# Performance work log

Measured on AMD Instinct MI355X. Metric: run time of the kernel, lower is better.

## Reference

```python
import jax, jax.numpy as jnp
import numpy as np

B, S, D, K, DF, H, DFF = 2, 512, 512, 8, 64, 8, 2048
DH = D // H  # d_head = 64
CS = D // K  # chunk_size = 64


def layer_norm(x, g, b, eps=1e-5):
    m = x.mean(-1, keepdims=True)
    v = ((x - m) ** 2).mean(-1, keepdims=True)
    return (x - m) / jnp.sqrt(v + eps) * g + b


def matexp_taylor(M, terms=6):
    # exp(M) ~= I + M + M^2/2! + ... (6 terms), batched over leading dims
    I = jnp.broadcast_to(jnp.eye(M.shape[-1], dtype=M.dtype), M.shape)
    res, P = I, I
    for n in range(1, terms + 1):
        P = jnp.matmul(P, M) / n
        res = res + P
    return res


def setup_inputs() -> dict:
    key = jax.random.key(0)
    ks = jax.random.split(key, 24)
    w = lambda k, shape, s=0.02: (jax.random.normal(k, shape, jnp.float32) * s)
    return {
        'x': jax.random.normal(ks[0], (B, S, D), jnp.float32),
        'u': jax.random.normal(ks[1], (B, S, DF), jnp.float32),
        'Wq': w(ks[2], (D, D)), 'bq': jnp.zeros((D,), jnp.float32),
        'Wk': w(ks[3], (D, D)), 'bk': jnp.zeros((D,), jnp.float32),
        'Wv': w(ks[4], (D, D)), 'bv': jnp.zeros((D,), jnp.float32),
        'Wo': w(ks[5], (D, D)), 'bo': jnp.zeros((D,), jnp.float32),
        'Wfp': w(ks[6], (DF, D)), 'bfp': jnp.zeros((D,), jnp.float32),
        'Wfo': w(ks[7], (D, DF)), 'bfo': jnp.zeros((DF,), jnp.float32),
        'Wc1': w(ks[8], (D, DFF)), 'bc1': jnp.zeros((DFF,), jnp.float32),
        'g_ln': jnp.ones((DFF,), jnp.float32), 'b_ln': jnp.zeros((DFF,), jnp.float32),
        # small scale keeps the Lie elements O(1) so the Taylor matexp is well-behaved
        'Wc2': w(ks[9], (DFF, D * K * K), 0.001), 'bc2': jnp.zeros((D * K * K,), jnp.float32),
    }


def reference(x, u, Wq, bq, Wk, bk, Wv, bv, Wo, bo, Wfp, bfp, Wfo, bfo,
              Wc1, bc1, g_ln, b_ln, Wc2, bc2):
    b, s, d = x.shape
    # --- ConnectionNetwork: A[b,s,d,k,k] ---
    h = jax.nn.gelu(x @ Wc1 + bc1, approximate=False)
    h = layer_norm(h, g_ln, b_ln)
    A = (h @ Wc2 + bc2).reshape(b, s, d, K, K)
    # --- ParallelTransport: lie[b,i,j] = sum_d (x_i - x_j)_d * A[j,d]  ---
    # (split into x_i.A_j and x_j.A_j terms to avoid [b,s,s,d,k,k] intermediate)
    lie = jnp.einsum('bid,bjdkl->bijkl', x, A) - jnp.einsum('bjd,bjdkl->bjkl', x, A)[:, None]
    Gamma = matexp_taylor(-lie)  # [b,s,s,k,k], Gamma[b,i,j] transports j->i
    # --- standard multi-head attention on x (eval mode, no dropout, no mask) ---
    q = (x @ Wq + bq).reshape(b, s, H, DH).transpose(0, 2, 1, 3)
    k_ = (x @ Wk + bk).reshape(b, s, H, DH).transpose(0, 2, 1, 3)
    v = (x @ Wv + bv).reshape(b, s, H, DH).transpose(0, 2, 1, 3)
    scores = jnp.einsum('bhid,bhjd->bhij', q, k_) / jnp.sqrt(jnp.float32(DH))
    attn = jax.nn.softmax(scores, axis=-1)
    ctx = jnp.einsum('bhij,bhjd->bhid', attn, v).transpose(0, 2, 1, 3).reshape(b, s, d)
    x_out = x + ctx @ Wo + bo
    # --- fiber transport: u_i += sum_j attn_avg[i,j] * Gamma[i,j] @ u_chunks[j] ---
    u_proj = u @ Wfp + bfp                      # [b,s,D]
    u_chunks = u_proj.reshape(b, s, K, CS)      # [b,s,k,cs]
    attn_avg = attn.mean(axis=1)                # [b,s,s]
    weighted = Gamma * attn_avg[..., None, None]
    u_t = jnp.einsum('bijkl,bjlc->bikc', weighted, u_chunks).reshape(b, s, d)
    u_out = u + u_t @ Wfo + bfo
    return (x_out, u_out)
```

## Files before the change

kernel.cpp:

```cpp
#include <hip/hip_runtime.h>
#include <math.h>

#define BB 2
#define SS 512
#define DD 512
#define HH 8
#define DFF 2048

typedef __attribute__((ext_vector_type(8))) short bf16x8;
typedef __attribute__((ext_vector_type(4))) float f32x4;

__device__ __forceinline__ float gelu_exact(float v) {
    return 0.5f * v * (1.0f + erff(v * 0.70710678118654752f));
}
__device__ __forceinline__ unsigned short f2bf(float f) {
    unsigned u = __float_as_uint(f);
    u += 0x7FFF + ((u >> 16) & 1);
    return (unsigned short)(u >> 16);
}
__device__ __forceinline__ float bf2f(unsigned short s) {
    return __uint_as_float(((unsigned)s) << 16);
}
__device__ __forceinline__ void gload16(const void* g, void* l) {
    __builtin_amdgcn_global_load_lds((const __attribute__((address_space(1))) void*)g,
                                     (__attribute__((address_space(3))) void*)l, 16, 0, 0);
}

template<int NT, int EPI>
__global__ __launch_bounds__(256)
void mgemm_k(const unsigned short* __restrict__ A, const unsigned short* __restrict__ B,
             const float* __restrict__ bias, const float* __restrict__ resid,
             float* __restrict__ Cf, unsigned short* __restrict__ Cb,
             int K, int lda, int ldb, int ldc, int batchH,
             long aSB, long aSH, long bSB, long bSH, long cSB, long cSH,
             float scale)
{
    __shared__ unsigned short As[128][32];
    __shared__ unsigned short Bs[NT][32];
    const int tid = threadIdx.x;
    const int wave = tid >> 6, lane = tid & 63;
    const int z = blockIdx.z;
    const int zb = z / batchH, zh = z % batchH;
    const unsigned short* Ab = A + (long)zb * aSB + (long)zh * aSH;
    const unsigned short* Bb = B + (long)zb * bSB + (long)zh * bSH;
    const int row0 = blockIdx.y * 128, col0 = blockIdx.x * NT;
    const int wm = wave >> 1, wn = wave & 1;
    const int lm = lane & 15, quad = lane >> 4;
    const int lrow = lane >> 2, lk = (lane & 3) * 8;
    constexpr int NTW = NT / 32;
    f32x4 acc[4][NTW];
    #pragma unroll
    for (int i = 0; i < 4; ++i)
        #pragma unroll
        for (int j = 0; j < NTW; ++j) acc[i][j] = (f32x4)0.f;

    for (int k0 = 0; k0 < K; k0 += 32) {
        #pragma unroll
        for (int t = 0; t < 2; ++t) {
            const int r = wave * 32 + t * 16;
            gload16(Ab + (long)(row0 + r + lrow) * lda + k0 + lk, &As[r][0]);
        }
        if (NT == 128) {
            #pragma unroll
            for (int t = 0; t < 2; ++t) {
                const int r = wave * 32 + t * 16;
                gload16(Bb + (long)(col0 + r + lrow) * ldb + k0 + lk, &Bs[r][0]);
            }
        } else {
            const int r = wave * 16;
            gload16(Bb + (long)(col0 + r + lrow) * ldb + k0 + lk, &Bs[r][0]);
        }
        __syncthreads();
        bf16x8 af[4], bfr[NTW];
        #pragma unroll
        for (int mt = 0; mt < 4; ++mt)
            af[mt] = *(const bf16x8*)&As[wm * 64 + mt * 16 + lm][quad * 8];
        #pragma unroll
        for (int nt = 0; nt < NTW; ++nt)
            bfr[nt] = *(const bf16x8*)&Bs[wn * (NT / 2) + nt * 16 + lm][quad * 8];
        #pragma unroll
        for (int mt = 0; mt < 4; ++mt)
            #pragma unroll
            for (int nt = 0; nt < NTW; ++nt)
                acc[mt][nt] = __builtin_amdgcn_mfma_f32_16x16x32_bf16(
                    af[mt], bfr[nt], acc[mt][nt], 0, 0, 0);
        __syncthreads();
    }
    float* Cfz = Cf ? Cf + (long)zb * cSB + (long)zh * cSH : nullptr;
    unsigned short* Cbz = Cb ? Cb + (long)zb * cSB + (long)zh * cSH : nullptr;
    #pragma unroll
    for (int mt = 0; mt < 4; ++mt) {
        #pragma unroll
        for (int nt = 0; nt < NTW; ++nt) {
            #pragma unroll
            for (int r = 0; r < 4; ++r) {
                const int row = row0 + wm * 64 + mt * 16 + quad * 4 + r;
                const int col = col0 + wn * (NT / 2) + nt * 16 + lm;
                float v = acc[mt][nt][r] * scale;
                if (EPI == 2)      v += bias[(col & 511) * 64 + (col >> 9)];
                else if (EPI == 1 || EPI == 4) v += bias[col];
                else if ((EPI == 3 || EPI == 5 || EPI == 6) && bias) v += bias[col];
                if (EPI == 1) v = gelu_exact(v);
                if (EPI == 4) v += resid[(long)row * ldc + col];
                if (EPI == 0 || EPI == 1 || EPI == 4)
                    Cfz[(long)row * ldc + col] = v;
                else if (EPI == 2 || EPI == 3)
                    Cbz[(long)row * ldc + col] = f2bf(v);
                else if (EPI == 5)
                    Cb[(long)(row >> 9) * 262144 + (col >> 6) * 32768 +
                       (col & 63) * 512 + (row & 511)] = f2bf(v);
                else if (EPI == 6)
                    Cb[(long)(row >> 9) * 262144 + (col & 63) * 4096 +
                       (row & 511) * 8 + (col >> 6)] = f2bf(v);
            }
        }
    }
}

__global__ __launch_bounds__(512, 2)
void fc2_k(const unsigned short* __restrict__ A, const unsigned short* __restrict__ Bm,
           const float* __restrict__ bias, unsigned short* __restrict__ C)
{
    extern __shared__ unsigned short smraw[];
#define SMH(buf, ab, h) (smraw + (((buf) * 4 + (ab) * 2 + (h)) * 8192))
    const int tid = threadIdx.x;
    const int wave = tid >> 6, lane = tid & 63;
    const int bid = blockIdx.x;
    const int lin = (bid & 7) * 64 + (bid >> 3);
    const int by = lin & 3, bx = lin >> 2;
    const int row0 = by * 256, col0 = bx * 256;
    const int wm = wave >> 2, wn = wave & 3;
    const int lm = lane & 15, quad = lane >> 4;
    const int axor = lm & 7;
    const int arow = (wm * 64 + lm) * 64;
    const int brow = (wn * 32 + lm) * 64;
    const int ca0 = ((quad) ^ axor) * 8;
    const int ca1 = ((quad + 4) ^ axor) * 8;
    const int srow = wave * 8 + (lane >> 3);
    const int scx = ((lane & 7) ^ ((lane >> 3) & 7)) * 8;
    const int sbrow = ((srow >> 5) << 6) + (srow & 31);
    const unsigned short* Ag = A + (long)(row0 + srow) * 2048 + scx;
    const unsigned short* Bg = Bm + (long)(col0 + sbrow) * 2048 + scx;

    f32x4 acc[8][4];
    #pragma unroll
    for (int i = 0; i < 8; ++i)
        #pragma unroll
        for (int j = 0; j < 4; ++j) acc[i][j] = (f32x4)0.f;
    bf16x8 afr[4][2], b0f[2][2], b1f[2][2];

#define STG(nb, ab, h, gp, HR) do { \
        const unsigned short* _g = (gp) + (h) * ((HR) * 2048); \
        unsigned short* _d = SMH(nb, ab, h) + wave * 512; \
        gload16(_g, _d); \
        gload16(_g + 128 * 2048, _d + 4096); \
    } while (0)
#define RDA(Hp) do { _Pragma("unroll") for (int _m = 0; _m < 4; ++_m) { \
        afr[_m][0] = *(const bf16x8*)((Hp) + arow + _m * 1024 + ca0); \
        afr[_m][1] = *(const bf16x8*)((Hp) + arow + _m * 1024 + ca1); } } while (0)
#define RDB(bf, Hp) do { _Pragma("unroll") for (int _n = 0; _n < 2; ++_n) { \
        bf[_n][0] = *(const bf16x8*)((Hp) + brow + _n * 1024 + ca0); \
        bf[_n][1] = *(const bf16x8*)((Hp) + brow + _n * 1024 + ca1); } } while (0)
#define MM(QM, QN, bf) do { _Pragma("unroll") for (int _m = 0; _m < 4; ++_m) \
        _Pragma("unroll") for (int _n = 0; _n < 2; ++_n) { \
        acc[(QM)*4+_m][(QN)*2+_n] = __builtin_amdgcn_mfma_f32_16x16x32_bf16( \
            afr[_m][0], bf[_n][0], acc[(QM)*4+_m][(QN)*2+_n], 0, 0, 0); \
        acc[(QM)*4+_m][(QN)*2+_n] = __builtin_amdgcn_mfma_f32_16x16x32_bf16( \
            afr[_m][1], bf[_n][1], acc[(QM)*4+_m][(QN)*2+_n], 0, 0, 0); } } while (0)
#define PH_MID() \
        __builtin_amdgcn_s_barrier(); \
        asm volatile("s_waitcnt lgkmcnt(0)" ::: "memory"); \
        __builtin_amdgcn_sched_barrier(0); \
        __builtin_amdgcn_s_setprio(1)
#define PH_END(VM) \
        __builtin_amdgcn_s_setprio(0); \
        __builtin_amdgcn_sched_barrier(0); \
        asm volatile("s_waitcnt vmcnt(" #VM ")" ::: "memory"); \
        __builtin_amdgcn_sched_barrier(0); \
        __builtin_amdgcn_s_barrier()
#define PH_END_NW() \
        __builtin_amdgcn_s_setprio(0); \
        __builtin_amdgcn_sched_barrier(0); \
        __builtin_amdgcn_s_barrier()

    STG(0, 0, 0, Ag, 64);
    STG(0, 1, 0, Bg, 32);
    STG(0, 1, 1, Bg, 32);
    STG(0, 0, 1, Ag, 64);
    Ag += 64; Bg += 64;
    asm volatile("s_waitcnt vmcnt(4)" ::: "memory");
    __builtin_amdgcn_s_barrier();

    #pragma unroll 1
    for (int t = 0; t < 31; ++t) {
        const int cur = t & 1, nb = cur ^ 1;
        const unsigned short* A0p = SMH(cur, 0, 0);
        const unsigned short* A1p = SMH(cur, 0, 1);
        const unsigned short* B0p = SMH(cur, 1, 0);
        const unsigned short* B1p = SMH(cur, 1, 1);
        RDA(A0p); RDB(b0f, B0p);
        STG(nb, 0, 0, Ag, 64);
        PH_MID(); MM(0, 0, b0f); PH_END(4);
        RDB(b1f, B1p);
        STG(nb, 1, 0, Bg, 32);
        PH_MID(); MM(0, 1, b1f); PH_END(4);
        RDA(A1p);
        STG(nb, 1, 1, Bg, 32);
        PH_MID(); MM(1, 1, b1f); PH_END_NW();
        STG(nb, 0, 1, Ag, 64);
        PH_MID(); MM(1, 0, b0f); PH_END(4);
        Ag += 64; Bg += 64;
    }
    {
        const unsigned short* A0p = SMH(1, 0, 0);
        const unsigned short* A1p = SMH(1, 0, 1);
        const unsigned short* B0p = SMH(1, 1, 0);
        const unsigned short* B1p = SMH(1, 1, 1);
        RDA(A0p); RDB(b0f, B0p);
        PH_MID(); MM(0, 0, b0f); PH_END(2);
        RDB(b1f, B1p);
        PH_MID(); MM(0, 1, b1f); PH_END(0);
        RDA(A1p);
        PH_MID(); MM(1, 1, b1f); PH_END_NW();
        PH_MID(); MM(1, 0, b0f); PH_END_NW();
    }

    const int crow = row0 + wm * 128 + quad * 4;
    const int ccol0 = col0 + wn * 64 + lm;
    #pragma unroll
    for (int ms = 0; ms < 8; ++ms)
        #pragma unroll
        for (int ns = 0; ns < 4; ++ns) {
            const int col = ccol0 + ns * 16;
            const float bv = bias[(col & 511) * 64 + (col >> 9)];
            #pragma unroll
            for (int r = 0; r < 4; ++r) {
                const int row = crow + ms * 16 + r;
                C[(long)row * 32768 + col] = f2bf(acc[ms][ns][r] + bv);
            }
        }
#undef SMH
#undef STG
#undef RDA
#undef RDB
#undef MM
#undef PH_MID
#undef PH_END
#undef PH_END_NW
}

__global__ __launch_bounds__(256)
void liegamma_k(const unsigned short* __restrict__ xb, const unsigned short* __restrict__ At,
                const float* __restrict__ xa, const float* __restrict__ aavg,
                unsigned short* __restrict__ Gw)
{
    __shared__ unsigned short Xs[128][32];
    __shared__ unsigned short Ts[64][32];
    __shared__ float Ml[128][68];
    const int tid = threadIdx.x;
    const int wave = tid >> 6, lane = tid & 63;
    const int b = blockIdx.z, j = blockIdx.y;
    const int i0 = blockIdx.x * 128;
    const int lm = lane & 15, quad = lane >> 4;
    const int lrow = lane >> 2, lk = (lane & 3) * 8;
    const unsigned short* Xb = xb + ((long)b * 512 + i0) * 512;
    const unsigned short* Tb = At + ((long)(b * 512 + j)) * 32768;
    f32x4 acc[2][4];
    #pragma unroll
    for (int i = 0; i < 2; ++i)
        #pragma unroll
        for (int n = 0; n < 4; ++n) acc[i][n] = (f32x4)0.f;

    for (int k0 = 0; k0 < 512; k0 += 32) {
        #pragma unroll
        for (int t = 0; t < 2; ++t) {
            const int r = wave * 32 + t * 16;
            gload16(Xb + (long)(r + lrow) * 512 + k0 + lk, &Xs[r][0]);
        }
        {
            const int r = wave * 16;
            gload16(Tb + (long)(r + lrow) * 512 + k0 + lk, &Ts[r][0]);
        }
        __syncthreads();
        bf16x8 af[2], bfr[4];
        #pragma unroll
        for (int mt = 0; mt < 2; ++mt)
            af[mt] = *(const bf16x8*)&Xs[wave * 32 + mt * 16 + lm][quad * 8];
        #pragma unroll
        for (int nt = 0; nt < 4; ++nt)
            bfr[nt] = *(const bf16x8*)&Ts[nt * 16 + lm][quad * 8];
        #pragma unroll
        for (int mt = 0; mt < 2; ++mt)
            #pragma unroll
            for (int nt = 0; nt < 4; ++nt)
                acc[mt][nt] = __builtin_amdgcn_mfma_f32_16x16x32_bf16(
                    af[mt], bfr[nt], acc[mt][nt], 0, 0, 0);
        __syncthreads();
    }
    const float* xar = xa + ((long)(b * 512 + j)) * 64;
    #pragma unroll
    for (int mt = 0; mt < 2; ++mt)
        #pragma unroll
        for (int nt = 0; nt < 4; ++nt) {
            const float xv = xar[nt * 16 + lm];
            #pragma unroll
            for (int r = 0; r < 4; ++r)
                Ml[wave * 32 + mt * 16 + quad * 4 + r][nt * 16 + lm] = xv - acc[mt][nt][r];
        }
    __syncthreads();
    const int r8 = tid & 7, mg = tid >> 3;
    #pragma unroll 1
    for (int pass = 0; pass < 4; ++pass) {
        const int mi = pass * 32 + mg;
        const f32x4* Mr = (const f32x4*)&Ml[mi][0];
        f32x4 Mreg[16];
        #pragma unroll
        for (int l = 0; l < 16; ++l) Mreg[l] = Mr[l];
        float P[8], res[8];
        #pragma unroll
        for (int c = 0; c < 8; ++c) { const float iv = (c == r8) ? 1.f : 0.f; P[c] = iv; res[c] = iv; }
        #pragma unroll
        for (int n = 1; n <= 6; ++n) {
            float tmp[8] = {0.f,0.f,0.f,0.f,0.f,0.f,0.f,0.f};
            const float invn = 1.f / (float)n;
            #pragma unroll
            for (int l = 0; l < 8; ++l) {
                const f32x4 m0 = Mreg[l * 2], m1 = Mreg[l * 2 + 1];
                const float pl = P[l];
                #pragma unroll
                for (int c = 0; c < 4; ++c) {
                    tmp[c]     = fmaf(pl, m0[c], tmp[c]);
                    tmp[4 + c] = fmaf(pl, m1[c], tmp[4 + c]);
                }
            }
            #pragma unroll
            for (int c = 0; c < 8; ++c) { P[c] = tmp[c] * invn; res[c] += P[c]; }
        }
        const float av = aavg[((long)b * 512 + i0 + mi) * 512 + j];
        bf16x8 o;
        #pragma unroll
        for (int c = 0; c < 8; ++c) o[c] = (short)f2bf(res[c] * av);
        *(bf16x8*)(Gw + ((long)(b * 8 + r8) * 512 + (i0 + mi)) * 4096 + (long)j * 8) = o;
    }
}

__global__ __launch_bounds__(256)
void lnbf_k(const float* __restrict__ h, const float* __restrict__ g,
            const float* __restrict__ b, unsigned short* __restrict__ out)
{
    const long row = blockIdx.x;
    const float* r = h + row * (long)DFF;
    const int tid = threadIdx.x;
    float vals[8];
    float s = 0.f, sq = 0.f;
    #pragma unroll
    for (int e = 0; e < 8; ++e) {
        const float v = r[tid + e * 256];
        vals[e] = v; s += v; sq += v * v;
    }
    __shared__ float rs[256], rq[256];
    rs[tid] = s; rq[tid] = sq; __syncthreads();
    for (int st = 128; st > 0; st >>= 1) {
        if (tid < st) { rs[tid] += rs[tid + st]; rq[tid] += rq[tid + st]; }
        __syncthreads();
    }
    const float mean = rs[0] * (1.f / DFF);
    const float var  = rq[0] * (1.f / DFF) - mean * mean;
    const float inv  = rsqrtf(var + 1e-5f);
    unsigned short* o = out + row * (long)DFF;
    #pragma unroll
    for (int e = 0; e < 8; ++e) {
        const int c = tid + e * 256;
        o[c] = f2bf((vals[e] - mean) * inv * g[c] + b[c]);
    }
}

__global__ __launch_bounds__(256)
void xa_k(const float* __restrict__ x, const unsigned short* __restrict__ At,
          float* __restrict__ xa)
{
    const int bj = blockIdx.x;
    const int tid = threadIdx.x;
    const int kl = tid >> 2, q = tid & 3;
    const unsigned short* Ar = At + (long)bj * 32768 + kl * 512 + q * 128;
    const float* xr = x + (long)bj * 512 + q * 128;
    float s = 0.f;
    #pragma unroll
    for (int d0 = 0; d0 < 128; d0 += 8) {
        const bf16x8 a = *(const bf16x8*)&Ar[d0];
        const f32x4 x0 = *(const f32x4*)&xr[d0];
        const f32x4 x1 = *(const f32x4*)&xr[d0 + 4];
        s = fmaf(x0[0], bf2f((unsigned short)a[0]), s);
        s = fmaf(x0[1], bf2f((unsigned short)a[1]), s);
        s = fmaf(x0[2], bf2f((unsigned short)a[2]), s);
        s = fmaf(x0[3], bf2f((unsigned short)a[3]), s);
        s = fmaf(x1[0], bf2f((unsigned short)a[4]), s);
        s = fmaf(x1[1], bf2f((unsigned short)a[5]), s);
        s = fmaf(x1[2], bf2f((unsigned short)a[6]), s);
        s = fmaf(x1[3], bf2f((unsigned short)a[7]), s);
    }
    __shared__ float red[64][5];
    red[kl][q] = s; __syncthreads();
    if (q == 0)
        xa[(long)bj * 64 + kl] = red[kl][0] + red[kl][1] + red[kl][2] + red[kl][3];
}

__global__ __launch_bounds__(256)
void softmax_k(float* __restrict__ p, unsigned short* __restrict__ pb)
{
    const long row = blockIdx.x;
    float* r = p + row * 512;
    const int tid = threadIdx.x;
    float v0 = r[tid], v1 = r[tid + 256];
    __shared__ float red[256];
    red[tid] = fmaxf(v0, v1); __syncthreads();
    for (int s = 128; s > 0; s >>= 1) {
        if (tid < s) red[tid] = fmaxf(red[tid], red[tid + s]);
        __syncthreads();
    }
    const float m = red[0]; __syncthreads();
    v0 = expf(v0 - m); v1 = expf(v1 - m);
    red[tid] = v0 + v1; __syncthreads();
    for (int s = 128; s > 0; s >>= 1) {
        if (tid < s) red[tid] += red[tid + s];
        __syncthreads();
    }
    const float inv = 1.f / red[0];
    const float a0 = v0 * inv, a1 = v1 * inv;
    r[tid] = a0; r[tid + 256] = a1;
    unsigned short* rb = pb + row * 512;
    rb[tid] = f2bf(a0); rb[tid + 256] = f2bf(a1);
}

__global__ __launch_bounds__(256)
void aavg_k(const float* __restrict__ attn, float* __restrict__ aavg)
{
    const long idx = (long)blockIdx.x * 256 + threadIdx.x;
    const int b = (int)(idx >> 18);
    const long rem = idx & 262143;
    float s = 0.f;
    #pragma unroll
    for (int h = 0; h < HH; ++h)
        s += attn[(long)b * 2097152 + (long)h * 262144 + rem];
    aavg[idx] = s * 0.125f;
}

__global__ __launch_bounds__(256)
void tconv_k(const float* __restrict__ in, unsigned short* __restrict__ out,
             int R, int C)
{
    __shared__ float Ls[64][65];
    const int c0 = blockIdx.x * 64, r0 = blockIdx.y * 64;
    const int tid = threadIdx.x;
    const int tc = tid & 63, tr = tid >> 6;
    #pragma unroll
    for (int p = 0; p < 16; ++p)
        Ls[tr + p * 4][tc] = in[(long)(r0 + tr + p * 4) * C + c0 + tc];
    __syncthreads();
    #pragma unroll
    for (int p = 0; p < 16; ++p)
        out[(long)(c0 + tr + p * 4) * R + r0 + tc] = f2bf(Ls[tc][tr + p * 4]);
}

__global__ __launch_bounds__(256)
void wc2p_k(const float* __restrict__ in, unsigned short* __restrict__ out)
{
    __shared__ float Ls[64][65];
    const int d0 = blockIdx.x;
    const long f0 = blockIdx.y * 64;
    const int tid = threadIdx.x;
    const int tc = tid & 63, tr = tid >> 6;
    #pragma unroll
    for (int p = 0; p < 16; ++p)
        Ls[tr + p * 4][tc] = in[(f0 + tr + p * 4) * 32768 + (long)d0 * 64 + tc];
    __syncthreads();
    #pragma unroll
    for (int p = 0; p < 16; ++p) {
        const int kl = tr + p * 4;
        out[((long)kl * 512 + d0) * 2048 + f0 + tc] = f2bf(Ls[tc][kl]);
    }
}

__global__ __launch_bounds__(256)
void f2bf_k(const float* __restrict__ in, unsigned short* __restrict__ out, int n)
{
    const int i = blockIdx.x * 256 + threadIdx.x;
    if (i < n) out[i] = f2bf(in[i]);
}

extern "C" void kernel_launch(void* const* d_in, const int* in_sizes, int n_in,
                              void* d_out, int out_size, void* d_ws, size_t ws_size,
                              hipStream_t stream) {
    const float* x   = (const float*)d_in[0];
    const float* u   = (const float*)d_in[1];
    const float* Wq  = (const float*)d_in[2];  const float* bq  = (const float*)d_in[3];
    const float* Wk  = (const float*)d_in[4];  const float* bk  = (const float*)d_in[5];
    const float* Wv  = (const float*)d_in[6];  const float* bv  = (const float*)d_in[7];
    const float* Wo  = (const float*)d_in[8];  const float* bo  = (const float*)d_in[9];
    const float* Wfp = (const float*)d_in[10]; const float* bfp = (const float*)d_in[11];
    const float* Wfo = (const float*)d_in[12]; const float* bfo = (const float*)d_in[13];
    const float* Wc1 = (const float*)d_in[14]; const float* bc1 = (const float*)d_in[15];
    const float* gln = (const float*)d_in[16]; const float* bln = (const float*)d_in[17];
    const float* Wc2 = (const float*)d_in[18]; const float* bc2 = (const float*)d_in[19];

    float* ws = (float*)d_ws;
    unsigned short* Wc2p = (unsigned short*)(ws);
    unsigned short* Gw   = (unsigned short*)(ws);
    unsigned short* At   = (unsigned short*)(ws + 33554432);
    float*          h    = ws + 50331648;
    unsigned short* h_bf = (unsigned short*)(ws + 52428800);
    unsigned short* x_bf = (unsigned short*)(ws + 53477376);
    unsigned short* u_bf = (unsigned short*)(ws + 53739520);
    unsigned short* Wc1t = (unsigned short*)(ws + 53772288);
    unsigned short* Wqt  = (unsigned short*)(ws + 54296576);
    unsigned short* Wkt  = (unsigned short*)(ws + 54427648);
    unsigned short* Wvt  = (unsigned short*)(ws + 54558720);
    unsigned short* Wot  = (unsigned short*)(ws + 54689792);
    unsigned short* Wfpt = (unsigned short*)(ws + 54820864);
    unsigned short* Wfot = (unsigned short*)(ws + 54837248);
    float*          xa   = ws + 54853632;
    unsigned short* q_bf = (unsigned short*)(ws + 54919168);
    unsigned short* k_bf = (unsigned short*)(ws + 55181312);
    unsigned short* vT   = (unsigned short*)(ws + 55443456);
    float*          sc   = ws + 55705600;
    unsigned short* at_bf= (unsigned short*)(ws + 59899904);
    float*          av   = ws + 61997056;
    unsigned short* ctx  = (unsigned short*)(ws + 62521344);
    unsigned short* upT2 = (unsigned short*)(ws + 62783488);
    unsigned short* ut_bf= (unsigned short*)(ws + 63045632);
    float* xout = (float*)d_out;
    float* uout = xout + 524288;

    const dim3 blk(256);

    hipFuncSetAttribute(reinterpret_cast<const void*>(fc2_k),
                        hipFuncAttributeMaxDynamicSharedMemorySize, 131072);

    tconv_k<<<dim3(32, 8), blk, 0, stream>>>(Wc1, Wc1t, 512, 2048);
    tconv_k<<<dim3(8, 8), blk, 0, stream>>>(Wq, Wqt, 512, 512);
    tconv_k<<<dim3(8, 8), blk, 0, stream>>>(Wk, Wkt, 512, 512);
    tconv_k<<<dim3(8, 8), blk, 0, stream>>>(Wv, Wvt, 512, 512);
    tconv_k<<<dim3(8, 8), blk, 0, stream>>>(Wo, Wot, 512, 512);
    tconv_k<<<dim3(8, 1), blk, 0, stream>>>(Wfp, Wfpt, 64, 512);
    tconv_k<<<dim3(1, 8), blk, 0, stream>>>(Wfo, Wfot, 512, 64);
    wc2p_k<<<dim3(512, 32), blk, 0, stream>>>(Wc2, Wc2p);
    f2bf_k<<<dim3(2048), blk, 0, stream>>>(x, x_bf, 524288);
    f2bf_k<<<dim3(256), blk, 0, stream>>>(u, u_bf, 65536);

    mgemm_k<128,3><<<dim3(4, 8, 1), blk, 0, stream>>>(
        x_bf, Wqt, bq, nullptr, nullptr, q_bf, 512, 512, 512, 512,
        1, 0,0,0,0,0,0, 1.0f);
    mgemm_k<128,3><<<dim3(4, 8, 1), blk, 0, stream>>>(
        x_bf, Wkt, bk, nullptr, nullptr, k_bf, 512, 512, 512, 512,
        1, 0,0,0,0,0,0, 1.0f);
    mgemm_k<128,5><<<dim3(4, 8, 1), blk, 0, stream>>>(
        x_bf, Wvt, bv, nullptr, nullptr, vT, 512, 512, 512, 512,
        1, 0,0,0,0,0,0, 1.0f);
    mgemm_k<128,0><<<dim3(4, 4, 16), blk, 0, stream>>>(
        q_bf, k_bf, nullptr, nullptr, sc, nullptr, 64, 512, 512, 512,
        8, 262144,64, 262144,64, 2097152,262144, 0.125f);
    softmax_k<<<dim3(BB * HH * SS), blk, 0, stream>>>(sc, at_bf);
    aavg_k<<<dim3(2048), blk, 0, stream>>>(sc, av);
    mgemm_k<64,3><<<dim3(1, 4, 16), blk, 0, stream>>>(
        at_bf, vT, nullptr, nullptr, nullptr, ctx, 512, 512, 512, 512,
        8, 2097152,262144, 262144,32768, 262144,64, 1.0f);
    mgemm_k<128,4><<<dim3(4, 8, 1), blk, 0, stream>>>(
        ctx, Wot, bo, x, xout, nullptr, 512, 512, 512, 512,
        1, 0,0,0,0,0,0, 1.0f);

    mgemm_k<128,1><<<dim3(16, 8, 1), blk, 0, stream>>>(
        x_bf, Wc1t, bc1, nullptr, h, nullptr, 512, 512, 512, 2048,
        1, 0,0,0,0,0,0, 1.0f);
    lnbf_k<<<dim3(1024), blk, 0, stream>>>(h, gln, bln, h_bf);
    fc2_k<<<dim3(512), dim3(512), 131072, stream>>>(h_bf, Wc2p, bc2, At);
    xa_k<<<dim3(1024), blk, 0, stream>>>(x, At, xa);
    liegamma_k<<<dim3(4, 512, 2), blk, 0, stream>>>(x_bf, At, xa, av, Gw);

    mgemm_k<128,6><<<dim3(4, 8, 1), blk, 0, stream>>>(
        u_bf, Wfpt, bfp, nullptr, nullptr, upT2, 64, 64, 64, 512,
        1, 0,0,0,0,0,0, 1.0f);
    mgemm_k<64,3><<<dim3(1, 4, 16), blk, 0, stream>>>(
        Gw, upT2, nullptr, nullptr, nullptr, ut_bf, 4096, 4096, 4096, 512,
        8, 16777216,2097152, 262144,0, 262144,64, 1.0f);
    mgemm_k<64,4><<<dim3(1, 8, 1), blk, 0, stream>>>(
        ut_bf, Wfot, bfo, u, uout, nullptr, 512, 512, 512, 64,
        1, 0,0,0,0,0,0, 1.0f);
}
```

Measured before the change: 942.5 us.

## Triple-buffer B tiles in fc2 GEMM with two-ahead prefetch

Restructures the fc2 GEMM main loop so A stays double-buffered but B tiles are triple-buffered and prefetched two K-steps ahead, with a rotating buffer index and adjusted vmcnt waits. The epilogue iteration is folded into the loop by clamping the prefetch index. The aim is to hide more global-load latency for the large weight operand. In exchange, dynamic LDS grows from 128KB to 160KB, which can cut occupancy from 2 blocks to 1 per CU. The clamped final iterations also issue redundant loads.

```diff
diff --git a/kernel.cpp b/kernel.cpp
--- a/kernel.cpp
+++ b/kernel.cpp
@@ -122,7 +122,8 @@
            const float* __restrict__ bias, unsigned short* __restrict__ C)
 {
     extern __shared__ unsigned short smraw[];
-#define SMH(buf, ab, h) (smraw + (((buf) * 4 + (ab) * 2 + (h)) * 8192))
+#define SMA(ab, h) (smraw + (((ab) * 2 + (h)) * 8192))
+#define SMB(bb, h) (smraw + (32768 + ((bb) * 2 + (h)) * 8192))
     const int tid = threadIdx.x;
     const int wave = tid >> 6, lane = tid & 63;
     const int bid = blockIdx.x;
@@ -139,8 +140,8 @@
     const int srow = wave * 8 + (lane >> 3);
     const int scx = ((lane & 7) ^ ((lane >> 3) & 7)) * 8;
     const int sbrow = ((srow >> 5) << 6) + (srow & 31);
-    const unsigned short* Ag = A + (long)(row0 + srow) * 2048 + scx;
-    const unsigned short* Bg = Bm + (long)(col0 + sbrow) * 2048 + scx;
+    const unsigned short* AgB = A + (long)(row0 + srow) * 2048 + scx;
+    const unsigned short* BgB = Bm + (long)(col0 + sbrow) * 2048 + scx;
 
     f32x4 acc[8][4];
     #pragma unroll
@@ -149,9 +150,15 @@
         for (int j = 0; j < 4; ++j) acc[i][j] = (f32x4)0.f;
     bf16x8 afr[4][2], b0f[2][2], b1f[2][2];
 
-#define STG(nb, ab, h, gp, HR) do { \
-        const unsigned short* _g = (gp) + (h) * ((HR) * 2048); \
-        unsigned short* _d = SMH(nb, ab, h) + wave * 512; \
+#define STGA(ab, h, toff) do { \
+        const unsigned short* _g = AgB + (toff) * 64 + (h) * (64 * 2048); \
+        unsigned short* _d = SMA(ab, h) + wave * 512; \
+        gload16(_g, _d); \
+        gload16(_g + 128 * 2048, _d + 4096); \
+    } while (0)
+#define STGB(bb, h, toff) do { \
+        const unsigned short* _g = BgB + (toff) * 64 + (h) * (32 * 2048); \
+        unsigned short* _d = SMB(bb, h) + wave * 512; \
         gload16(_g, _d); \
         gload16(_g + 128 * 2048, _d + 4096); \
     } while (0)
@@ -183,47 +190,40 @@
         __builtin_amdgcn_sched_barrier(0); \
         __builtin_amdgcn_s_barrier()
 
-    STG(0, 0, 0, Ag, 64);
-    STG(0, 1, 0, Bg, 32);
-    STG(0, 1, 1, Bg, 32);
-    STG(0, 0, 1, Ag, 64);
-    Ag += 64; Bg += 64;
-    asm volatile("s_waitcnt vmcnt(4)" ::: "memory");
+    STGB(0, 0, 0);
+    STGB(0, 1, 0);
+    STGA(0, 0, 0);
+    STGA(0, 1, 0);
+    STGB(1, 0, 1);
+    STGB(1, 1, 1);
+    asm volatile("s_waitcnt vmcnt(6)" ::: "memory");
     __builtin_amdgcn_s_barrier();
 
+    int rA = 0;
+    int rB = 0, mB = 1, wB = 2;
     #pragma unroll 1
-    for (int t = 0; t < 31; ++t) {
-        const int cur = t & 1, nb = cur ^ 1;
-        const unsigned short* A0p = SMH(cur, 0, 0);
-        const unsigned short* A1p = SMH(cur, 0, 1);
-        const unsigned short* B0p = SMH(cur, 1, 0);
-        const unsigned short* B1p = SMH(cur, 1, 1);
+    for (int t = 0; t < 32; ++t) {
+        const int tA = (t + 1 < 32) ? (t + 1) : 31;
+        const int tB = (t + 2 < 32) ? (t + 2) : 31;
+        const unsigned short* A0p = SMA(rA, 0);
+        const unsigned short* A1p = SMA(rA, 1);
+        const unsigned short* B0p = SMB(rB, 0);
+        const unsigned short* B1p = SMB(rB, 1);
         RDA(A0p); RDB(b0f, B0p);
-        STG(nb, 0, 0, Ag, 64);
-        PH_MID(); MM(0, 0, b0f); PH_END(4);
+        STGA(rA ^ 1, 0, tA);
+        PH_MID(); MM(0, 0, b0f); PH_END_NW();
         RDB(b1f, B1p);
-        STG(nb, 1, 0, Bg, 32);
-        PH_MID(); MM(0, 1, b1f); PH_END(4);
+        STGA(rA ^ 1, 1, tA);
+        PH_MID(); MM(0, 1, b1f); PH_END(8);
         RDA(A1p);
-        STG(nb, 1, 1, Bg, 32);
+        STGB(wB, 0, tB);
         PH_MID(); MM(1, 1, b1f); PH_END_NW();
-        STG(nb, 0, 1, Ag, 64);
-        PH_MID(); MM(1, 0, b0f); PH_END(4);
-        Ag += 64; Bg += 64;
-    }
-    {
-        const unsigned short* A0p = SMH(1, 0, 0);
-        const unsigned short* A1p = SMH(1, 0, 1);
-        const unsigned short* B0p = SMH(1, 1, 0);
-        const unsigned short* B1p = SMH(1, 1, 1);
-        RDA(A0p); RDB(b0f, B0p);
-        PH_MID(); MM(0, 0, b0f); PH_END(2);
-        RDB(b1f, B1p);
-        PH_MID(); MM(0, 1, b1f); PH_END(0);
-        RDA(A1p);
-        PH_MID(); MM(1, 1, b1f); PH_END_NW();
-        PH_MID(); MM(1, 0, b0f); PH_END_NW();
-    }
+        STGB(wB, 1, tB);
+        PH_MID(); MM(1, 0, b0f); PH_END(6);
+        rA ^= 1;
+        const int tmp = rB; rB = mB; mB = wB; wB = tmp;
+    }
+    asm volatile("s_waitcnt vmcnt(0)" ::: "memory");
 
     const int crow = row0 + wm * 128 + quad * 4;
     const int ccol0 = col0 + wn * 64 + lm;
@@ -239,8 +239,10 @@
                 C[(long)row * 32768 + col] = f2bf(acc[ms][ns][r] + bv);
             }
         }
-#undef SMH
-#undef STG
+#undef SMA
+#undef SMB
+#undef STGA
+#undef STGB
 #undef RDA
 #undef RDB
 #undef MM
@@ -534,7 +536,7 @@
     const dim3 blk(256);
 
     hipFuncSetAttribute(reinterpret_cast<const void*>(fc2_k),
-                        hipFuncAttributeMaxDynamicSharedMemorySize, 131072);
+                        hipFuncAttributeMaxDynamicSharedMemorySize, 163840);
 
     tconv_k<<<dim3(32, 8), blk, 0, stream>>>(Wc1, Wc1t, 512, 2048);
     tconv_k<<<dim3(8, 8), blk, 0, stream>>>(Wq, Wqt, 512, 512);
@@ -572,7 +574,7 @@
         x_bf, Wc1t, bc1, nullptr, h, nullptr, 512, 512, 512, 2048,
         1, 0,0,0,0,0,0, 1.0f);
     lnbf_k<<<dim3(1024), blk, 0, stream>>>(h, gln, bln, h_bf);
-    fc2_k<<<dim3(512), dim3(512), 131072, stream>>>(h_bf, Wc2p, bc2, At);
+    fc2_k<<<dim3(512), dim3(512), 163840, stream>>>(h_bf, Wc2p, bc2, At);
     xa_k<<<dim3(1024), blk, 0, stream>>>(x, At, xa);
     liegamma_k<<<dim3(4, 512, 2), blk, 0, stream>>>(x_bf, At, xa, av, Gw);
 
```

Result: no change. 944.1 us (+0.2%).
